# Kernel optimization log

Measured on AMD Instinct MI355X. Metric: run time of the kernel, lower is better.

## Reference

```python
import jax, jax.numpy as jnp
from jax import lax
import numpy as np

L, DIRS, H, D_IN, B, T = 2, 2, 512, 1024, 64, 512


def setup_inputs() -> dict:
    key = jax.random.key(0)
    ks = jax.random.split(key, 6)
    s = 1.0 / np.sqrt(H)  # pytorch LSTM init scale
    return {
        "seq": jax.random.normal(ks[0], (B, T, D_IN), dtype=jnp.float32),
        "mask": jnp.zeros((B, T), dtype=jnp.int32),  # no padding -> else branch
        "w_ih": jax.random.normal(ks[1], (L, DIRS, 4 * H, D_IN), dtype=jnp.float32) * s,
        "w_hh": jax.random.normal(ks[2], (L, DIRS, 4 * H, H), dtype=jnp.float32) * s,
        "b_ih": jax.random.normal(ks[3], (L, DIRS, 4 * H), dtype=jnp.float32) * s,
        "b_hh": jax.random.normal(ks[4], (L, DIRS, 4 * H), dtype=jnp.float32) * s,
    }


def _run_dir(x, wi, wh, bi, bh, reverse):
    # x: [T, B, D]; wi: [4H, D]; wh: [4H, H]
    xg = jnp.einsum("tbd,gd->tbg", x, wi) + bi + bh  # precompute input gates [T,B,4H]
    if reverse:
        xg = xg[::-1]
    bsz = x.shape[1]
    h0 = jnp.zeros((bsz, H), x.dtype)

    def step(carry, g_t):
        h, c = carry
        g = g_t + h @ wh.T
        i, f, gg, o = jnp.split(g, 4, axis=-1)  # pytorch gate order i,f,g,o
        i = jax.nn.sigmoid(i)
        f = jax.nn.sigmoid(f)
        gg = jnp.tanh(gg)
        o = jax.nn.sigmoid(o)
        c = f * c + i * gg
        h = o * jnp.tanh(c)
        return (h, c), h

    _, hs = lax.scan(step, (h0, h0), xg)  # [T,B,H]
    if reverse:
        hs = hs[::-1]
    return hs


def reference(seq, mask, w_ih, w_hh, b_ih, b_hh):
    # mask is all zeros (no padding): plain full-length bidirectional LSTM
    x = jnp.transpose(seq, (1, 0, 2))  # [T, B, D]
    for l in range(L):
        fwd = _run_dir(x, w_ih[l, 0], w_hh[l, 0], b_ih[l, 0], b_hh[l, 0], False)
        bwd = _run_dir(x, w_ih[l, 1], w_hh[l, 1], b_ih[l, 1], b_hh[l, 1], True)
        x = jnp.concatenate([fwd, bwd], axis=-1)  # [T, B, 2H]
    return jnp.transpose(x, (1, 0, 2))  # [B, T, 2H]
```

## Files before the change

### kernel.cpp

```cpp
#include <hip/hip_runtime.h>
#include <cstdint>

typedef unsigned short u16;
typedef __attribute__((ext_vector_type(8))) short short8;
typedef __attribute__((ext_vector_type(4))) short short4v;
typedef __attribute__((ext_vector_type(4))) float f32x4;


__device__ __forceinline__ u16 f2bf(float x){
  uint32_t u = __float_as_uint(x);
  u += 0x7fffu + ((u >> 16) & 1u);
  return (u16)(u >> 16);
}
__device__ __forceinline__ float bf2f(u16 b){ return __uint_as_float(((uint32_t)b) << 16); }
__device__ __forceinline__ float sigm(float x){ return 1.f / (1.f + __expf(-x)); }
__device__ __forceinline__ float tanhx(float x){
  float xc = fminf(fmaxf(x, -30.f), 30.f);
  float e  = __expf(-2.f * xc);
  return (1.f - e) / (1.f + e);
}

__device__ __forceinline__ void st4_l2(u16* p, uint32_t v){
  asm volatile("global_store_dword %0, %1, off sc0" :: "v"(p), "v"(v) : "memory");
}

#define CNT_STRIDE 16

__global__ void k_cvt(const float* __restrict__ in, u16* __restrict__ out, int n4){
  int i = blockIdx.x * blockDim.x + threadIdx.x;
  if (i >= n4) return;
  float4 v = ((const float4*)in)[i];
  ushort4 o;
  o.x = f2bf(v.x); o.y = f2bf(v.y); o.z = f2bf(v.z); o.w = f2bf(v.w);
  ((ushort4*)out)[i] = o;
}

template<int LAYER0>
__global__ __launch_bounds__(256) void k_gemm(
    const u16* __restrict__ A, const u16* __restrict__ W,
    const float* __restrict__ bih, const float* __restrict__ bhh,
    u16* __restrict__ xg)
{
  __shared__ u16 Al[128 * 64];
  __shared__ u16 Bl[128 * 64];
  const int tid  = threadIdx.x;
  const int bm   = blockIdx.x, bn = blockIdx.y;
  const int w    = tid >> 6, lane = tid & 63;
  const int wm   = (w >> 1) * 64;
  const int wn   = (w & 1) * 64;
  f32x4 acc[4][4] = {};

  for (int kt = 0; kt < 1024; kt += 64){
    __syncthreads();
    #pragma unroll
    for (int it = 0; it < 4; ++it){
      int idx = tid + it * 256;
      int row = idx >> 3, c = idx & 7;
      size_t aoff;
      int m = bm * 128 + row;
      if (LAYER0) aoff = ((size_t)(m & 63) * 512 + (m >> 6)) * 1024;
      else        aoff = (size_t)m * 1024;
      short8 va = *(const short8*)(A + aoff + kt + c * 8);
      *(short8*)(Al + row * 64 + ((c ^ (row & 7)) * 8)) = va;
      int n = bn * 128 + row;
      short8 vb = *(const short8*)(W + (size_t)n * 1024 + kt + c * 8);
      *(short8*)(Bl + row * 64 + ((c ^ (row & 7)) * 8)) = vb;
    }
    __syncthreads();
    const int kg = lane >> 4;
    #pragma unroll
    for (int kk = 0; kk < 2; ++kk){
      short8 a[4], b[4];
      #pragma unroll
      for (int i = 0; i < 4; ++i){
        int rA = wm + i * 16 + (lane & 15);
        int cA = kk * 4 + kg;
        a[i] = *(const short8*)(Al + rA * 64 + ((cA ^ (rA & 7)) * 8));
        int rB = wn + i * 16 + (lane & 15);
        b[i] = *(const short8*)(Bl + rB * 64 + ((cA ^ (rB & 7)) * 8));
      }
      #pragma unroll
      for (int i = 0; i < 4; ++i)
        #pragma unroll
        for (int j = 0; j < 4; ++j)
          acc[i][j] = __builtin_amdgcn_mfma_f32_16x16x32_bf16(a[i], b[j], acc[i][j], 0, 0, 0);
    }
  }
  #pragma unroll
  for (int i = 0; i < 4; ++i){
    #pragma unroll
    for (int j = 0; j < 4; ++j){
      int n_g = bn * 128 + wn + j * 16 + (lane & 15);
      float bias = bih[n_g] + bhh[n_g];
      #pragma unroll
      for (int q = 0; q < 4; ++q){
        int m_g = bm * 128 + wm + i * 16 + (lane >> 4) * 4 + q;
        xg[(size_t)m_g * 4096 + n_g] = f2bf(acc[i][j][q] + bias);
      }
    }
  }
}

template<int LAYER>
__global__ __launch_bounds__(256, 1) void k_rec(
    const u16* __restrict__ whh,
    const u16* __restrict__ xg,
    u16*  __restrict__ x1,
    u16*  __restrict__ hexch,
    float* __restrict__ dout,
    int*  __restrict__ ctrl,
    int*  __restrict__ cnt)
{
  const int tid = threadIdx.x;
  __shared__ int sh_rank, sh_grp;

  if (tid == 0){
    uint32_t xcd;
    asm volatile("s_getreg_b32 %0, hwreg(HW_REG_XCC_ID)" : "=s"(xcd));
    xcd &= 7;
    int rank = __hip_atomic_fetch_add(ctrl + xcd * 16, 1, __ATOMIC_RELAXED, __HIP_MEMORY_SCOPE_AGENT);
    int dm;
    if (rank == 0){
      int slot = __hip_atomic_fetch_add(ctrl + 136, 1, __ATOMIC_RELAXED, __HIP_MEMORY_SCOPE_AGENT);
      dm = slot + 1;
      __hip_atomic_store(ctrl + 128 + xcd, dm, __ATOMIC_RELEASE, __HIP_MEMORY_SCOPE_AGENT);
    } else {
      do {
        dm = __hip_atomic_load(ctrl + 128 + xcd, __ATOMIC_ACQUIRE, __HIP_MEMORY_SCOPE_AGENT);
      } while (dm == 0);
    }
    sh_rank = rank; sh_grp = dm - 1;
  }
  __syncthreads();
  const int s   = sh_rank;
  const int grp = sh_grp;
  if (s >= 32 || grp >= 4) return;
  const int dir = grp >> 1, bh = grp & 1;

  const int w    = tid >> 6, lane = tid & 63;
  const int aj   = lane & 15;
  const int kg   = lane >> 4;

  __shared__ u16  h_lds[64 * 512];
  __shared__ float gates_lds[4][64][17];

  const u16* wd = whh + (size_t)dir * (2048 * 512);
  short8 bq[16];
  {
    const size_t rbase = (size_t)(w * 512 + s * 16 + aj) * 512;
    #pragma unroll
    for (int kk = 0; kk < 16; ++kk)
      bq[kk] = *(const short8*)(wd + rbase + kk * 32 + kg * 8);
  }

  float cst[2] = {0.f, 0.f};
  const int tstep = dir ? -1 : 1;
  const int t0    = dir ? 511 : 0;
  int* const cntd = cnt + (size_t)grp * 512 * CNT_STRIDE;

  const int gm = tid >> 3;
  const int j0 = (tid & 7) * 2;
  const int b  = bh * 32 + gm;

  for (int it = 0; it < 512; ++it){
    const int t = t0 + tstep * it;

    const size_t xb0 = ((size_t)t * 64 + b) * 4096 + (size_t)dir * 2048 + s * 16 + j0;
    ushort2 xgv[4];
    #pragma unroll
    for (int g = 0; g < 4; ++g) xgv[g] = *(const ushort2*)(xg + xb0 + g * 512);

    f32x4 acc0 = {0.f,0.f,0.f,0.f}, acc1 = {0.f,0.f,0.f,0.f};

    if (it > 0){
      const int tprev = t - tstep;
      if (tid == 0){
        int* cp = cntd + (it - 1) * CNT_STRIDE;
        const int zero = 0;
        while (true){
          int old;
          asm volatile("global_atomic_add %0, %1, %2, off sc0\n\ts_waitcnt vmcnt(0)"
                       : "=v"(old) : "v"(cp), "v"(zero) : "memory");
          if (old >= 32) break;
          __builtin_amdgcn_s_sleep(1);
        }
      }
      __syncthreads();

      const u16* hsrc;
      size_t rstride;
      if (LAYER == 0){ hsrc = x1 + ((size_t)tprev * 64 + bh * 32) * 1024 + dir * 512; rstride = 1024; }
      else           { hsrc = hexch + ((size_t)tprev * 4 + grp) * (32 * 512);          rstride = 512; }

      short8 hv[8];
      #pragma unroll
      for (int i = 0; i < 8; ++i){
        int ii  = (i + s) & 7;
        int idx = ii * 256 + tid;
        int row = idx >> 6, c = idx & 63;
        const u16* src = hsrc + (size_t)row * rstride + c * 8;
        asm volatile("global_load_dwordx4 %0, %1, off sc0" : "=v"(hv[i]) : "v"(src));
      }
      asm volatile("s_waitcnt vmcnt(4)" ::: "memory");
      __builtin_amdgcn_sched_barrier(0);
      #pragma unroll
      for (int i = 0; i < 4; ++i){
        int ii  = (i + s) & 7;
        int idx = ii * 256 + tid;
        int row = idx >> 6, c = idx & 63;
        *(short8*)(h_lds + row * 512 + ((c ^ (row & 7)) * 8)) = hv[i];
      }
      asm volatile("s_waitcnt vmcnt(0)" ::: "memory");
      __builtin_amdgcn_sched_barrier(0);
      #pragma unroll
      for (int i = 4; i < 8; ++i){
        int ii  = (i + s) & 7;
        int idx = ii * 256 + tid;
        int row = idx >> 6, c = idx & 63;
        *(short8*)(h_lds + row * 512 + ((c ^ (row & 7)) * 8)) = hv[i];
      }
      __syncthreads();

      #pragma unroll
      for (int kk = 0; kk < 16; ++kk){
        int c = kk * 4 + kg;
        short8 a0 = *(const short8*)(h_lds + aj * 512 + ((c ^ (aj & 7)) * 8));
        int r1 = 16 + aj;
        short8 a1 = *(const short8*)(h_lds + r1 * 512 + ((c ^ (r1 & 7)) * 8));
        acc0 = __builtin_amdgcn_mfma_f32_16x16x32_bf16(a0, bq[kk], acc0, 0, 0, 0);
        acc1 = __builtin_amdgcn_mfma_f32_16x16x32_bf16(a1, bq[kk], acc1, 0, 0, 0);
      }
    }

    #pragma unroll
    for (int q = 0; q < 4; ++q){
      gates_lds[w][kg * 4 + q][aj]      = acc0[q];
      gates_lds[w][16 + kg * 4 + q][aj] = acc1[q];
    }
    __syncthreads();

    uint32_t hpack;
    float hof[2];
    #pragma unroll
    for (int q = 0; q < 2; ++q){
      const int j = j0 + q;
      float gi = gates_lds[0][gm][j] + bf2f(((const u16*)&xgv[0])[q]);
      float gf = gates_lds[1][gm][j] + bf2f(((const u16*)&xgv[1])[q]);
      float gg = gates_lds[2][gm][j] + bf2f(((const u16*)&xgv[2])[q]);
      float go = gates_lds[3][gm][j] + bf2f(((const u16*)&xgv[3])[q]);
      float iv = sigm(gi), fv = sigm(gf), gv = tanhx(gg), ov = sigm(go);
      float c  = fv * cst[q] + iv * gv;
      cst[q]   = c;
      float h  = ov * tanhx(c);
      hof[q]   = h;
      if (q == 0) hpack = (uint32_t)f2bf(h);
      else        hpack |= ((uint32_t)f2bf(h)) << 16;
    }

    if (LAYER == 0){
      u16* dst = x1 + ((size_t)t * 64 + b) * 1024 + dir * 512 + s * 16 + j0;
      st4_l2(dst, hpack);
      asm volatile("s_waitcnt vmcnt(0)" ::: "memory");
    } else {
      u16* dst = hexch + ((size_t)t * 4 + grp) * (32 * 512) + gm * 512 + s * 16 + j0;
      st4_l2(dst, hpack);
      float2 dv = { hof[0], hof[1] };
      *(float2*)(dout + ((size_t)b * 512 + t) * 1024 + dir * 512 + s * 16 + j0) = dv;
      asm volatile("s_waitcnt vmcnt(1)" ::: "memory");
    }
    __syncthreads();
    if (tid == 0){
      int* cp = cntd + it * CNT_STRIDE;
      const int one = 1;
      asm volatile("global_atomic_add %0, %1, off" :: "v"(cp), "v"(one) : "memory");
    }
  }
}

extern "C" void kernel_launch(void* const* d_in, const int* in_sizes, int n_in,
                              void* d_out, int out_size, void* d_ws, size_t ws_size,
                              hipStream_t stream){
  (void)in_sizes; (void)n_in; (void)out_size; (void)ws_size;
  const float* seq = (const float*)d_in[0];
  const float* wih = (const float*)d_in[2];
  const float* whh = (const float*)d_in[3];
  const float* bih = (const float*)d_in[4];
  const float* bhh = (const float*)d_in[5];
  float* out = (float*)d_out;

  char* ws    = (char*)d_ws;
  int*  ctrl0 = (int*)ws;
  int*  ctrl1 = ctrl0 + 256;
  int*  cnt0  = ctrl0 + 512;
  int*  cnt1  = cnt0 + 32768;

  u16*  seqb = (u16*)(ws + 524288);
  u16*  wihb = seqb + (size_t)33554432;
  u16*  whhb = wihb + (size_t)8388608;
  u16*  x1   = whhb + (size_t)4194304;
  u16*  xgb  = x1   + (size_t)33554432;
  u16*  hexb = seqb;

  hipMemsetAsync(ctrl0, 0, 266240, stream);
  k_cvt<<<32768, 256, 0, stream>>>(seq, seqb, 8388608);
  k_cvt<<<8192,  256, 0, stream>>>(wih, wihb, 2097152);
  k_cvt<<<4096,  256, 0, stream>>>(whh, whhb, 1048576);

  dim3 gg(256, 32);
  k_gemm<1><<<gg, 256, 0, stream>>>(seqb, wihb, bih, bhh, xgb);
  k_rec<0><<<512, 256, 0, stream>>>(whhb, xgb, x1, hexb, out, ctrl0, cnt0);
  k_gemm<0><<<gg, 256, 0, stream>>>(x1, wihb + 4194304, bih + 4096, bhh + 4096, xgb);
  k_rec<1><<<512, 256, 0, stream>>>(whhb + 2097152, xgb, x1, hexb, out, ctrl1, cnt1);
}
```

Baseline: 3.899 ms.

## Split recurrent batch into quarters to spread LSTM recurrence over all XCDs

The persistent recurrent kernel now splits each direction's batch into four 16-row quarters instead of two 32-row halves. That gives 8 groups of 32 cooperating blocks instead of 4, so all XCDs take part. Each block now loads half as many h rows per step and runs one MFMA accumulation chain, split into two interleaved accumulators, instead of two. The intent is to shorten the per-timestep critical path of the serial recurrence. In exchange, each thread writes one 16-bit value with narrower stores, and the counter workspace and memset size are doubled to cover the extra groups.

```diff
diff --git a/kernel.cpp b/kernel.cpp
--- a/kernel.cpp
+++ b/kernel.cpp
@@ -3,7 +3,6 @@
 
 typedef unsigned short u16;
 typedef __attribute__((ext_vector_type(8))) short short8;
-typedef __attribute__((ext_vector_type(4))) short short4v;
 typedef __attribute__((ext_vector_type(4))) float f32x4;
 
 
@@ -20,8 +19,8 @@
   return (1.f - e) / (1.f + e);
 }
 
-__device__ __forceinline__ void st4_l2(u16* p, uint32_t v){
-  asm volatile("global_store_dword %0, %1, off sc0" :: "v"(p), "v"(v) : "memory");
+__device__ __forceinline__ void st2_l2(u16* p, uint32_t v){
+  asm volatile("global_store_short %0, %1, off sc0" :: "v"(p), "v"(v) : "memory");
 }
 
 #define CNT_STRIDE 16
@@ -134,8 +133,8 @@
   __syncthreads();
   const int s   = sh_rank;
   const int grp = sh_grp;
-  if (s >= 32 || grp >= 4) return;
-  const int dir = grp >> 1, bh = grp & 1;
+  if (s >= 32 || grp >= 8) return;
+  const int dir = grp >> 2, bq = grp & 3;
 
   const int w    = tid >> 6, lane = tid & 63;
   const int aj   = lane & 15;
@@ -145,32 +144,32 @@
   __shared__ float gates_lds[4][64][17];
 
   const u16* wd = whh + (size_t)dir * (2048 * 512);
-  short8 bq[16];
+  short8 bq_[16];
   {
     const size_t rbase = (size_t)(w * 512 + s * 16 + aj) * 512;
     #pragma unroll
     for (int kk = 0; kk < 16; ++kk)
-      bq[kk] = *(const short8*)(wd + rbase + kk * 32 + kg * 8);
-  }
-
-  float cst[2] = {0.f, 0.f};
+      bq_[kk] = *(const short8*)(wd + rbase + kk * 32 + kg * 8);
+  }
+
+  float cst = 0.f;
   const int tstep = dir ? -1 : 1;
   const int t0    = dir ? 511 : 0;
   int* const cntd = cnt + (size_t)grp * 512 * CNT_STRIDE;
 
-  const int gm = tid >> 3;
-  const int j0 = (tid & 7) * 2;
-  const int b  = bh * 32 + gm;
+  const int gm = tid >> 4;
+  const int j  = tid & 15;
+  const int b  = bq * 16 + gm;
 
   for (int it = 0; it < 512; ++it){
     const int t = t0 + tstep * it;
 
-    const size_t xb0 = ((size_t)t * 64 + b) * 4096 + (size_t)dir * 2048 + s * 16 + j0;
-    ushort2 xgv[4];
-    #pragma unroll
-    for (int g = 0; g < 4; ++g) xgv[g] = *(const ushort2*)(xg + xb0 + g * 512);
-
-    f32x4 acc0 = {0.f,0.f,0.f,0.f}, acc1 = {0.f,0.f,0.f,0.f};
+    const size_t xb0 = ((size_t)t * 64 + b) * 4096 + (size_t)dir * 2048 + s * 16 + j;
+    u16 xgv[4];
+    #pragma unroll
+    for (int g = 0; g < 4; ++g) xgv[g] = xg[xb0 + g * 512];
+
+    f32x4 accA = {0.f,0.f,0.f,0.f}, accB = {0.f,0.f,0.f,0.f};
 
     if (it > 0){
       const int tprev = t - tstep;
@@ -189,23 +188,23 @@
 
       const u16* hsrc;
       size_t rstride;
-      if (LAYER == 0){ hsrc = x1 + ((size_t)tprev * 64 + bh * 32) * 1024 + dir * 512; rstride = 1024; }
-      else           { hsrc = hexch + ((size_t)tprev * 4 + grp) * (32 * 512);          rstride = 512; }
-
-      short8 hv[8];
-      #pragma unroll
-      for (int i = 0; i < 8; ++i){
-        int ii  = (i + s) & 7;
+      if (LAYER == 0){ hsrc = x1 + ((size_t)tprev * 64 + bq * 16) * 1024 + dir * 512; rstride = 1024; }
+      else           { hsrc = hexch + ((size_t)tprev * 8 + grp) * (16 * 512);          rstride = 512; }
+
+      short8 hv[4];
+      #pragma unroll
+      for (int i = 0; i < 4; ++i){
+        int ii  = (i + s) & 3;
         int idx = ii * 256 + tid;
         int row = idx >> 6, c = idx & 63;
         const u16* src = hsrc + (size_t)row * rstride + c * 8;
         asm volatile("global_load_dwordx4 %0, %1, off sc0" : "=v"(hv[i]) : "v"(src));
       }
-      asm volatile("s_waitcnt vmcnt(4)" ::: "memory");
+      asm volatile("s_waitcnt vmcnt(2)" ::: "memory");
       __builtin_amdgcn_sched_barrier(0);
       #pragma unroll
-      for (int i = 0; i < 4; ++i){
-        int ii  = (i + s) & 7;
+      for (int i = 0; i < 2; ++i){
+        int ii  = (i + s) & 3;
         int idx = ii * 256 + tid;
         int row = idx >> 6, c = idx & 63;
         *(short8*)(h_lds + row * 512 + ((c ^ (row & 7)) * 8)) = hv[i];
@@ -213,8 +212,8 @@
       asm volatile("s_waitcnt vmcnt(0)" ::: "memory");
       __builtin_amdgcn_sched_barrier(0);
       #pragma unroll
-      for (int i = 4; i < 8; ++i){
-        int ii  = (i + s) & 7;
+      for (int i = 2; i < 4; ++i){
+        int ii  = (i + s) & 3;
         int idx = ii * 256 + tid;
         int row = idx >> 6, c = idx & 63;
         *(short8*)(h_lds + row * 512 + ((c ^ (row & 7)) * 8)) = hv[i];
@@ -224,48 +223,37 @@
       #pragma unroll
       for (int kk = 0; kk < 16; ++kk){
         int c = kk * 4 + kg;
-        short8 a0 = *(const short8*)(h_lds + aj * 512 + ((c ^ (aj & 7)) * 8));
-        int r1 = 16 + aj;
-        short8 a1 = *(const short8*)(h_lds + r1 * 512 + ((c ^ (r1 & 7)) * 8));
-        acc0 = __builtin_amdgcn_mfma_f32_16x16x32_bf16(a0, bq[kk], acc0, 0, 0, 0);
-        acc1 = __builtin_amdgcn_mfma_f32_16x16x32_bf16(a1, bq[kk], acc1, 0, 0, 0);
-      }
-    }
-
-    #pragma unroll
-    for (int q = 0; q < 4; ++q){
-      gates_lds[w][kg * 4 + q][aj]      = acc0[q];
-      gates_lds[w][16 + kg * 4 + q][aj] = acc1[q];
-    }
+        short8 a = *(const short8*)(h_lds + aj * 512 + ((c ^ (aj & 7)) * 8));
+        if (kk & 1) accB = __builtin_amdgcn_mfma_f32_16x16x32_bf16(a, bq_[kk], accB, 0, 0, 0);
+        else        accA = __builtin_amdgcn_mfma_f32_16x16x32_bf16(a, bq_[kk], accA, 0, 0, 0);
+      }
+      #pragma unroll
+      for (int q = 0; q < 4; ++q) accA[q] += accB[q];
+    }
+
+    #pragma unroll
+    for (int q = 0; q < 4; ++q)
+      gates_lds[w][kg * 4 + q][aj] = accA[q];
     __syncthreads();
 
-    uint32_t hpack;
-    float hof[2];
-    #pragma unroll
-    for (int q = 0; q < 2; ++q){
-      const int j = j0 + q;
-      float gi = gates_lds[0][gm][j] + bf2f(((const u16*)&xgv[0])[q]);
-      float gf = gates_lds[1][gm][j] + bf2f(((const u16*)&xgv[1])[q]);
-      float gg = gates_lds[2][gm][j] + bf2f(((const u16*)&xgv[2])[q]);
-      float go = gates_lds[3][gm][j] + bf2f(((const u16*)&xgv[3])[q]);
-      float iv = sigm(gi), fv = sigm(gf), gv = tanhx(gg), ov = sigm(go);
-      float c  = fv * cst[q] + iv * gv;
-      cst[q]   = c;
-      float h  = ov * tanhx(c);
-      hof[q]   = h;
-      if (q == 0) hpack = (uint32_t)f2bf(h);
-      else        hpack |= ((uint32_t)f2bf(h)) << 16;
-    }
+    float gi = gates_lds[0][gm][j] + bf2f(xgv[0]);
+    float gf = gates_lds[1][gm][j] + bf2f(xgv[1]);
+    float gg = gates_lds[2][gm][j] + bf2f(xgv[2]);
+    float go = gates_lds[3][gm][j] + bf2f(xgv[3]);
+    float iv = sigm(gi), fv = sigm(gf), gv = tanhx(gg), ov = sigm(go);
+    float c  = fv * cst + iv * gv;
+    cst      = c;
+    float h  = ov * tanhx(c);
+    uint32_t hb16 = (uint32_t)f2bf(h);
 
     if (LAYER == 0){
-      u16* dst = x1 + ((size_t)t * 64 + b) * 1024 + dir * 512 + s * 16 + j0;
-      st4_l2(dst, hpack);
+      u16* dst = x1 + ((size_t)t * 64 + b) * 1024 + dir * 512 + s * 16 + j;
+      st2_l2(dst, hb16);
       asm volatile("s_waitcnt vmcnt(0)" ::: "memory");
     } else {
-      u16* dst = hexch + ((size_t)t * 4 + grp) * (32 * 512) + gm * 512 + s * 16 + j0;
-      st4_l2(dst, hpack);
-      float2 dv = { hof[0], hof[1] };
-      *(float2*)(dout + ((size_t)b * 512 + t) * 1024 + dir * 512 + s * 16 + j0) = dv;
+      u16* dst = hexch + ((size_t)t * 8 + grp) * (16 * 512) + gm * 512 + s * 16 + j;
+      st2_l2(dst, hb16);
+      dout[((size_t)b * 512 + t) * 1024 + dir * 512 + s * 16 + j] = h;
       asm volatile("s_waitcnt vmcnt(1)" ::: "memory");
     }
     __syncthreads();
@@ -292,16 +280,16 @@
   int*  ctrl0 = (int*)ws;
   int*  ctrl1 = ctrl0 + 256;
   int*  cnt0  = ctrl0 + 512;
-  int*  cnt1  = cnt0 + 32768;
-
-  u16*  seqb = (u16*)(ws + 524288);
+  int*  cnt1  = cnt0 + 65536;
+
+  u16*  seqb = (u16*)(ws + 786432);
   u16*  wihb = seqb + (size_t)33554432;
   u16*  whhb = wihb + (size_t)8388608;
   u16*  x1   = whhb + (size_t)4194304;
   u16*  xgb  = x1   + (size_t)33554432;
   u16*  hexb = seqb;
 
-  hipMemsetAsync(ctrl0, 0, 266240, stream);
+  hipMemsetAsync(ctrl0, 0, 526336, stream);
   k_cvt<<<32768, 256, 0, stream>>>(seq, seqb, 8388608);
   k_cvt<<<8192,  256, 0, stream>>>(wih, wihb, 2097152);
   k_cvt<<<4096,  256, 0, stream>>>(whh, whhb, 1048576);
```

After: 3.278 ms. -15.9%, faster.
